# Optimization experiments

Measured on AMD Instinct MI355X. Metric: run time of the kernel, lower is better.

## Reference

```python
import jax, jax.numpy as jnp
import numpy as np

N = 50000
E = 1600000
D = 128
NUM_CLASSES = 10
SLOPE = 0.01  # torch leaky_relu default


def leaky_relu(x):
    return jnp.where(x >= 0, x, SLOPE * x)


def gcn_conv(x, src, dst, norm_out, norm_in, W, b):
    # DGL GraphConv, norm='both': D_out^{-1/2} A^T D_in^{-1/2} applied as
    # scale-src -> scatter-sum to dst -> scale-dst, then linear + bias.
    h = x * norm_out[:, None]                        # [N, D]
    agg = jax.ops.segment_sum(h[src], dst, num_segments=N)  # [N, D]
    agg = agg * norm_in[:, None]
    return agg @ W + b


def setup_inputs() -> dict:
    key = jax.random.key(0)
    ks = jax.random.split(key, 12)
    def w(k, shape, fan_in):
        return jax.random.normal(k, shape, dtype=jnp.float32) / np.sqrt(fan_in)
    return {
        "x": jax.random.normal(ks[0], (N, D), dtype=jnp.float32),
        "src": jax.random.randint(ks[1], (E,), 0, N),
        "dst": jax.random.randint(ks[2], (E,), 0, N),
        "W1": w(ks[3], (D, D), D),
        "b1": jnp.zeros((D,), jnp.float32),
        "W2": w(ks[4], (D, D), D),
        "b2": jnp.zeros((D,), jnp.float32),
        "agg_w": w(ks[5], (D, 1), D),
        "agg_b": jnp.zeros((1,), jnp.float32),
        "d1_w": w(ks[6], (N, 100), N),
        "d1_b": jnp.zeros((100,), jnp.float32),
        "d2_w": w(ks[7], (100, 20), 100),
        "d2_b": jnp.zeros((20,), jnp.float32),
        "d3_w": w(ks[8], (20, NUM_CLASSES), 20),
        "d3_b": jnp.zeros((NUM_CLASSES,), jnp.float32),
    }


def reference(x, src, dst, W1, b1, W2, b2, agg_w, agg_b,
              d1_w, d1_b, d2_w, d2_b, d3_w, d3_b):
    ones = jnp.ones((E,), jnp.float32)
    out_deg = jax.ops.segment_sum(ones, src, num_segments=N)
    in_deg = jax.ops.segment_sum(ones, dst, num_segments=N)
    # DGL clamps degrees to min 1 (allow_zero_in_degree path)
    norm_out = jnp.power(jnp.clip(out_deg, 1.0), -0.5)
    norm_in = jnp.power(jnp.clip(in_deg, 1.0), -0.5)

    h = gcn_conv(x, src, dst, norm_out, norm_in, W1, b1)
    h = leaky_relu(h)
    h = gcn_conv(h, src, dst, norm_out, norm_in, W2, b2)
    h = h @ agg_w + agg_b            # [N, 1]
    # dropout omitted (eval mode / identity)
    h = h.reshape(-1, N)             # [1, N]
    h = h @ d1_w + d1_b              # [1, 100]
    h = leaky_relu(h @ d2_w + d2_b)  # [1, 20]
    h = h @ d3_w + d3_b              # [1, num_classes]
    return h.reshape(1, -1)
```

## Files before the change

### kernel.cpp

```cpp
#include <hip/hip_runtime.h>
#include <hip/hip_bf16.h>

#define SLOPE 0.01f
#define D 128
#define CAP 64
#define NB 256
#define NPMAX 1024
#define ZB 512
#define ZIT 10

__device__ __forceinline__ float us2f(unsigned int u) {
    union { unsigned int i; float f; } c; c.i = u << 16; return c.f;
}
__device__ __forceinline__ unsigned int f2us(float f) {
    union { float f; unsigned int i; } c; c.f = f;
    return (c.i + 0x7fffu + ((c.i >> 16) & 1u)) >> 16;
}

__global__ void __launch_bounds__(256) k_hist782(const int* __restrict__ dst,
                                                 unsigned int* __restrict__ histg,
                                                 unsigned int* __restrict__ odeg,
                                                 int E, int NP, int N) {
    __shared__ int lb[NPMAX];
    int b = blockIdx.x;
    for (int i = b * 256 + threadIdx.x; i < N; i += NB * 256) odeg[i] = 0u;
    for (int i = threadIdx.x; i < NP; i += 256) lb[i] = 0;
    __syncthreads();
    int ch = (E + NB - 1) / NB;
    int e0 = b * ch, e1 = min(E, e0 + ch);
    for (int e = e0 + threadIdx.x; e < e1; e += 256) atomicAdd(&lb[dst[e] >> 6], 1);
    __syncthreads();
    unsigned int* row = histg + (size_t)b * NP;
    for (int i = threadIdx.x; i < NP; i += 256) row[i] = (unsigned int)lb[i];
}

__global__ void __launch_bounds__(NB) k_scanA(const unsigned int* __restrict__ histg,
                                              unsigned int* __restrict__ boffT,
                                              unsigned int* __restrict__ tot, int NP) {
    __shared__ int wsum[NB / 64];
    int p = blockIdx.x, tid = threadIdx.x, lane = tid & 63, w = tid >> 6;
    int val = (int)histg[(size_t)tid * NP + p];
    int sc = val;
    for (int off = 1; off < 64; off <<= 1) { int t = __shfl_up(sc, off, 64); if (lane >= off) sc += t; }
    if (lane == 63) wsum[w] = sc;
    __syncthreads();
    if (w == 0 && lane < NB / 64) {
        int v4 = wsum[lane];
        for (int off = 1; off < NB / 64; off <<= 1) { int t = __shfl_up(v4, off, 64); if (lane >= off) v4 += t; }
        wsum[lane] = v4;
    }
    __syncthreads();
    int excl = ((w == 0) ? 0 : wsum[w - 1]) + sc - val;
    boffT[(size_t)p * NB + tid] = (unsigned int)excl;
    if (tid == NB - 1) tot[p] = (unsigned int)(excl + val);
}

__global__ void __launch_bounds__(1024) k_misc(const unsigned int* __restrict__ tot,
                                               int* __restrict__ pbase, int NP,
                                               const float* __restrict__ W2, const float* __restrict__ b2,
                                               const float* __restrict__ agg_w, const float* __restrict__ agg_b,
                                               float* __restrict__ v, float* __restrict__ c) {
    __shared__ int wsum[16];
    __shared__ float aw[D];
    __shared__ float red[D];
    int tid = threadIdx.x;
    if (blockIdx.x == 0) {
        int lane = tid & 63, w = tid >> 6;
        int val = (tid < NP) ? (int)tot[tid] : 0;
        int sc = val;
        for (int off = 1; off < 64; off <<= 1) { int t = __shfl_up(sc, off, 64); if (lane >= off) sc += t; }
        if (lane == 63) wsum[w] = sc;
        __syncthreads();
        if (w == 0 && lane < 16) {
            int v16 = wsum[lane];
            for (int off = 1; off < 16; off <<= 1) { int t = __shfl_up(v16, off, 64); if (lane >= off) v16 += t; }
            wsum[lane] = v16;
        }
        __syncthreads();
        int excl = ((w == 0) ? 0 : wsum[w - 1]) + sc - val;
        if (tid <= NP) pbase[tid] = excl;
    } else {
        if (tid >= 128) return;
        aw[tid] = agg_w[tid];
        __syncthreads();
        float acc = 0.f;
        for (int j = 0; j < D; j++) acc += W2[tid * D + j] * aw[j];
        v[tid] = acc;
        red[tid] = b2[tid] * aw[tid];
        __syncthreads();
        for (int off = 64; off > 0; off >>= 1) {
            if (tid < off) red[tid] += red[tid + off];
            __syncthreads();
        }
        if (tid == 0) c[0] = red[0] + agg_b[0];
    }
}

__global__ void __launch_bounds__(256) k_psort(const int* __restrict__ src, const int* __restrict__ dst,
                                               const int* __restrict__ pbase,
                                               const unsigned int* __restrict__ boffT,
                                               unsigned int* __restrict__ parted,
                                               unsigned int* __restrict__ odeg, int E, int NP) {
    __shared__ unsigned int lbase[NPMAX];
    __shared__ int lcur[NPMAX];
    int b = blockIdx.x;
    for (int i = threadIdx.x; i < NP; i += 256) {
        lbase[i] = (unsigned int)pbase[i] + boffT[(size_t)i * NB + b];
        lcur[i] = 0;
    }
    __syncthreads();
    int ch = (E + NB - 1) / NB;
    int e0 = b * ch, e1 = min(E, e0 + ch);
    for (int e = e0 + threadIdx.x; e < e1; e += 256) {
        int d = dst[e], s = src[e];
        atomicAdd(&odeg[s], 1u);
        int p = d >> 6;
        int pos = atomicAdd(&lcur[p], 1);
        parted[lbase[p] + pos] = (unsigned int)s | ((unsigned int)(d & 63) << 16);
    }
}

__global__ void __launch_bounds__(256) k_bfill(
    const int* __restrict__ poff, const unsigned int* __restrict__ parted,
    unsigned short* __restrict__ bucket, int* __restrict__ cnt_in,
    float* __restrict__ norm_in, int N) {
    __shared__ int lcnt[64];
    __shared__ unsigned short blds[64 * CAP];
    int p = blockIdx.x, tid = threadIdx.x;
    if (tid < 64) lcnt[tid] = 0;
    __syncthreads();
    int e0 = poff[p], e1 = poff[p + 1];
    for (int i = e0 + tid; i < e1; i += 256) {
        unsigned int rec = parted[i];
        int dl = rec >> 16;
        int pos = atomicAdd(&lcnt[dl], 1);
        if (pos < CAP) blds[dl * CAP + pos] = (unsigned short)(rec & 0xffffu);
    }
    __syncthreads();
    int nmax = min(64, N - (p << 6));
    unsigned int* bg = (unsigned int*)(bucket + ((long)p << 6) * CAP);
    const unsigned int* bl = (const unsigned int*)blds;
    for (int i = tid; i < nmax * (CAP / 2); i += 256) bg[i] = bl[i];
    if (tid < nmax) {
        cnt_in[(p << 6) + tid] = lcnt[tid];
        norm_in[(p << 6) + tid] = rsqrtf(fmaxf((float)lcnt[tid], 1.0f));
    }
}

__global__ void k_prep(const float2* __restrict__ x2, const unsigned int* __restrict__ odeg,
                       unsigned int* __restrict__ xb, int total ) {
    int g = blockIdx.x * blockDim.x + threadIdx.x;
    if (g >= total) return;
    float no = rsqrtf(fmaxf((float)odeg[g >> 6], 1.0f));
    float2 p = x2[g];
    xb[g] = f2us(p.x * no) | (f2us(p.y * no) << 16);
}

__global__ void __launch_bounds__(256) k_gather1(
    const int* __restrict__ cnt_in, const unsigned short* __restrict__ bucket,
    const unsigned int* __restrict__ xb, unsigned int* __restrict__ agg, int N) {
    int b = blockIdx.x;
    int xcd = b & 7;
    int pass = xcd >> 1;
    int idx = ((b >> 3) << 1) + (xcd & 1);
    int tid = threadIdx.x;
    int node = idx * 4 + (tid >> 6);
    if (node >= N) return;
    int lane = tid & 63;
    int slot = lane >> 4;
    int fu = lane & 15;
    int deg = min(__builtin_nontemporal_load(cnt_in + node), CAP);
    int myedge = 0;
    if (lane < deg) myedge = (int)__builtin_nontemporal_load(bucket + (long)node * CAP + lane);
    const unsigned int* xq = xb + (size_t)(pass << 4) + fu;
    float ax = 0.f, ay = 0.f;
    {
        unsigned int pv[8];
#pragma unroll
        for (int i = 0; i < 8; i++) {
            int s = __shfl(myedge, i * 4 + slot, 64);
            pv[i] = xq[(size_t)s << 6];
        }
#pragma unroll
        for (int i = 0; i < 8; i++) {
            bool ok = (i * 4 + slot) < deg;
            ax += ok ? us2f(pv[i] & 0xffffu) : 0.f;
            ay += ok ? us2f(pv[i] >> 16) : 0.f;
        }
    }
    if (deg > 32) {
        unsigned int pv[8];
#pragma unroll
        for (int i = 0; i < 8; i++) {
            int s = __shfl(myedge, 32 + i * 4 + slot, 64);
            pv[i] = xq[(size_t)s << 6];
        }
#pragma unroll
        for (int i = 0; i < 8; i++) {
            bool ok = (32 + i * 4 + slot) < deg;
            ax += ok ? us2f(pv[i] & 0xffffu) : 0.f;
            ay += ok ? us2f(pv[i] >> 16) : 0.f;
        }
    }
    ax += __shfl_xor(ax, 16, 64); ay += __shfl_xor(ay, 16, 64);
    ax += __shfl_xor(ax, 32, 64); ay += __shfl_xor(ay, 32, 64);
    if (slot == 0)
        __builtin_nontemporal_store(f2us(ax) | (f2us(ay) << 16),
                                    agg + (long)node * 64 + (pass << 4) + fu);
}

__global__ void __launch_bounds__(256) k_lin1q(
    const unsigned int* __restrict__ agg, const float* __restrict__ W1,
    const float* __restrict__ b1, const float* __restrict__ v,
    const unsigned int* __restrict__ odeg, const float* __restrict__ norm_in,
    float* __restrict__ q, int N) {
    __shared__ __align__(16) unsigned int at[64 * 64];
    int tid = threadIdx.x;
    int cg = tid & 31;
    int rg = tid >> 5;
    int r0 = blockIdx.x * 64;

    {
        const uint4* ag4 = (const uint4*)agg;
        uint4* at4 = (uint4*)at;
        uint4 z4; z4.x = z4.y = z4.z = z4.w = 0u;
#pragma unroll
        for (int it = 0; it < 4; it++) {
            int idx = tid + it * 256;
            int r = idx >> 4;
            at4[idx] = (r0 + r < N) ? ag4[(long)(r0 + r) * 16 + (idx & 15)] : z4;
        }
    }
    __syncthreads();

    float4 acc[8];
#pragma unroll
    for (int i = 0; i < 8; i++) acc[i].x = acc[i].y = acc[i].z = acc[i].w = 0.f;

    const float4* W4 = (const float4*)W1;
    const uint4* a4 = ((const uint4*)at) + rg * 8 * 16;
    for (int kq = 0; kq < 16; kq++) {
        float4 w0 = W4[(kq * 8 + 0) * 32 + cg];
        float4 w1 = W4[(kq * 8 + 1) * 32 + cg];
        float4 w2 = W4[(kq * 8 + 2) * 32 + cg];
        float4 w3 = W4[(kq * 8 + 3) * 32 + cg];
        float4 w4 = W4[(kq * 8 + 4) * 32 + cg];
        float4 w5 = W4[(kq * 8 + 5) * 32 + cg];
        float4 w6 = W4[(kq * 8 + 6) * 32 + cg];
        float4 w7 = W4[(kq * 8 + 7) * 32 + cg];
#pragma unroll
        for (int i = 0; i < 8; i++) {
            uint4 a = a4[i * 16 + kq];
            float f0 = us2f(a.x & 0xffffu), f1 = us2f(a.x >> 16);
            float f2 = us2f(a.y & 0xffffu), f3 = us2f(a.y >> 16);
            float f4 = us2f(a.z & 0xffffu), f5 = us2f(a.z >> 16);
            float f6 = us2f(a.w & 0xffffu), f7 = us2f(a.w >> 16);
            acc[i].x += f0*w0.x + f1*w1.x + f2*w2.x + f3*w3.x + f4*w4.x + f5*w5.x + f6*w6.x + f7*w7.x;
            acc[i].y += f0*w0.y + f1*w1.y + f2*w2.y + f3*w3.y + f4*w4.y + f5*w5.y + f6*w6.y + f7*w7.y;
            acc[i].z += f0*w0.z + f1*w1.z + f2*w2.z + f3*w3.z + f4*w4.z + f5*w5.z + f6*w6.z + f7*w7.z;
            acc[i].w += f0*w0.w + f1*w1.w + f2*w2.w + f3*w3.w + f4*w4.w + f5*w5.w + f6*w6.w + f7*w7.w;
        }
    }

    float4 bv = ((const float4*)b1)[cg];
    float4 vv = ((const float4*)v)[cg];
#pragma unroll
    for (int i = 0; i < 8; i++) {
        int row = r0 + rg * 8 + i;
        bool valid = row < N;
        float ni = valid ? norm_in[row] : 0.f;
        float hx = ni * acc[i].x + bv.x; hx = hx >= 0.f ? hx : SLOPE * hx;
        float hy = ni * acc[i].y + bv.y; hy = hy >= 0.f ? hy : SLOPE * hy;
        float hz = ni * acc[i].z + bv.z; hz = hz >= 0.f ? hz : SLOPE * hz;
        float hw = ni * acc[i].w + bv.w; hw = hw >= 0.f ? hw : SLOPE * hw;
        float p = hx * vv.x + hy * vv.y + hz * vv.z + hw * vv.w;
        p += __shfl_down(p, 16, 32);
        p += __shfl_down(p, 8, 32);
        p += __shfl_down(p, 4, 32);
        p += __shfl_down(p, 2, 32);
        p += __shfl_down(p, 1, 32);
        if ((tid & 31) == 0 && valid)
            q[row] = rsqrtf(fmaxf((float)odeg[row], 1.0f)) * p;
    }
}

__global__ void __launch_bounds__(256) k_gather2(
    const int* __restrict__ cnt_in, const unsigned short* __restrict__ bucket,
    const float* __restrict__ q, const float* __restrict__ norm_in,
    const float* __restrict__ c, float* __restrict__ s, int N) {
    int tid = threadIdx.x;
    int node = blockIdx.x * 8 + (tid >> 5);
    int lane = tid & 31;
    if (node >= N) return;
    int deg = min(cnt_in[node], CAP);
    float t = 0.f;
    for (int j = lane; j < deg; j += 32) t += q[(int)bucket[(long)node * CAP + j]];
    t += __shfl_down(t, 16, 32);
    t += __shfl_down(t, 8, 32);
    t += __shfl_down(t, 4, 32);
    t += __shfl_down(t, 2, 32);
    t += __shfl_down(t, 1, 32);
    if (lane == 0) s[node] = norm_in[node] * t + c[0];
}

__global__ void __launch_bounds__(256) k_z1(const float* __restrict__ s,
                                            const float* __restrict__ d1w,
                                            float* __restrict__ zpart, int N) {
    __shared__ float ls[ZIT * 10];
    __shared__ float4 part[256];
    int tid = threadIdx.x;
    int qd = tid % 25;
    int rl = tid / 25;
    int rows_per = (N + gridDim.x - 1) / gridDim.x;
    int r0 = blockIdx.x * rows_per;
    int r1 = min(N, r0 + rows_per);
    if (tid < ZIT * 10) ls[tid] = (r0 + tid < r1) ? s[r0 + tid] : 0.f;
    __syncthreads();
    const float4* w4 = (const float4*)d1w;
    float4 acc; acc.x = acc.y = acc.z = acc.w = 0.f;
    if (tid < 250) {
#pragma unroll
        for (int it = 0; it < ZIT; it++) {
            int ro = rl + it * 10;
            float sv = ls[ro];
            int rr = min(r0 + ro, N - 1);
            float4 w = w4[(long)rr * 25 + qd];
            acc.x += sv * w.x; acc.y += sv * w.y; acc.z += sv * w.z; acc.w += sv * w.w;
        }
    }
    part[tid] = acc;
    __syncthreads();
    if (tid < 25) {
        float4 t = part[tid];
#pragma unroll
        for (int g = 1; g < 10; g++) {
            float4 p = part[tid + 25 * g];
            t.x += p.x; t.y += p.y; t.z += p.z; t.w += p.w;
        }
        ((float4*)zpart)[blockIdx.x * 25 + tid] = t;
    }
}

__global__ void __launch_bounds__(256) k_zred(const float* __restrict__ zpart,
                                              float* __restrict__ z1) {
    int gid = blockIdx.x * 256 + threadIdx.x;
    int col = gid >> 6;
    int lane = gid & 63;
    if (col >= 100) return;
    float sum = 0.f;
#pragma unroll
    for (int i = 0; i < ZB / 64; i++) {
        int b = lane * (ZB / 64) + i;
        sum += zpart[(size_t)b * 100 + col];
    }
    for (int off = 32; off > 0; off >>= 1) sum += __shfl_down(sum, off, 64);
    if (lane == 0) z1[col] = sum;
}

__global__ void k_head(const float* __restrict__ z1, const float* __restrict__ d1b,
                       const float* __restrict__ d2w, const float* __restrict__ d2b,
                       const float* __restrict__ d3w, const float* __restrict__ d3b,
                       float* __restrict__ out) {
    __shared__ float z1c[100];
    __shared__ float z2c[20];
    int tid = threadIdx.x;
    for (int i = tid; i < 100; i += 64) z1c[i] = z1[i] + d1b[i];
    __syncthreads();
    if (tid < 20) {
        float acc = d2b[tid];
        for (int k = 0; k < 100; k++) acc += z1c[k] * d2w[k * 20 + tid];
        z2c[tid] = acc >= 0.f ? acc : SLOPE * acc;
    }
    __syncthreads();
    if (tid < 10) {
        float acc = d3b[tid];
        for (int j = 0; j < 20; j++) acc += z2c[j] * d3w[j * 10 + tid];
        out[tid] = acc;
    }
}

extern "C" void kernel_launch(void* const* d_in, const int* in_sizes, int n_in,
                              void* d_out, int out_size, void* d_ws, size_t ws_size,
                              hipStream_t stream) {
    const int N = in_sizes[0] / D;
    const int E = in_sizes[1];
    const int NP = (N + 63) >> 6;

    const float* x     = (const float*)d_in[0];
    const int* src     = (const int*)d_in[1];
    const int* dst     = (const int*)d_in[2];
    const float* W1    = (const float*)d_in[3];
    const float* b1    = (const float*)d_in[4];
    const float* W2    = (const float*)d_in[5];
    const float* b2    = (const float*)d_in[6];
    const float* agg_w = (const float*)d_in[7];
    const float* agg_b = (const float*)d_in[8];
    const float* d1w   = (const float*)d_in[9];
    const float* d1b   = (const float*)d_in[10];
    const float* d2w   = (const float*)d_in[11];
    const float* d2b   = (const float*)d_in[12];
    const float* d3w   = (const float*)d_in[13];
    const float* d3b   = (const float*)d_in[14];
    float* out = (float*)d_out;

    unsigned int* xb  = (unsigned int*)d_ws;
    unsigned int* agg = xb + (size_t)N * 64;
    unsigned int* parted = agg;
    unsigned int* histg  = agg + E;
    unsigned int* boffT  = histg + (size_t)NB * NP;
    unsigned int* tot    = boffT + (size_t)NP * NB;
    unsigned int* odeg   = agg + (size_t)N * 64;
    float* norm_in    = (float*)(odeg + N);
    float* q          = norm_in + N;
    float* s          = q + N;
    float* v          = s + N;
    float* c          = v + 128;
    float* z1         = c + 4;
    int* pbase        = (int*)(z1 + 128);
    int* cnt_in       = pbase + NP + 16;
    unsigned short* bucket = (unsigned short*)(cnt_in + N);
    float* zpart      = (float*)(bucket + (size_t)N * CAP);


    k_hist782<<<NB, 256, 0, stream>>>(dst, histg, odeg, E, NP, N);
    k_scanA<<<NP, NB, 0, stream>>>(histg, boffT, tot, NP);
    k_misc<<<2, 1024, 0, stream>>>(tot, pbase, NP, W2, b2, agg_w, agg_b, v, c);
    k_psort<<<NB, 256, 0, stream>>>(src, dst, pbase, boffT, parted, odeg, E, NP);
    k_bfill<<<NP, 256, 0, stream>>>(pbase, parted, bucket, cnt_in, norm_in, N);
    k_prep<<<(N * 64 + 255) / 256, 256, 0, stream>>>((const float2*)x, odeg, xb, N * 64);

    {
        const int G = (N + 3) / 4;
        const int G2 = (G + 1) / 2;
        k_gather1<<<8 * G2, 256, 0, stream>>>(cnt_in, bucket, xb, agg, N);
    }
    k_lin1q<<<(N + 63) / 64, 256, 0, stream>>>(agg, W1, b1, v, odeg, norm_in, q, N);
    k_gather2<<<(N + 7) / 8, 256, 0, stream>>>(cnt_in, bucket, q, norm_in, c, s, N);
    k_z1<<<ZB, 256, 0, stream>>>(s, d1w, zpart, N);
    k_zred<<<25, 256, 0, stream>>>(zpart, z1);
    k_head<<<1, 64, 0, stream>>>(z1, d1b, d2w, d2b, d3w, d3b, out);
}
```

Baseline: 363.0 us.

## Split xb into per-pass planes with zero sentinel row and fuse tail kernels

The bf16 feature buffer is rearranged so each of the four 16-word feature passes has its own contiguous plane of N+1 rows, and an extra all-zero sentinel row is added. Bucket slots are pre-filled with the sentinel index, so the gather can drop its per-edge validity masks and the conditional bucket load. Each pass in k_gather1 now reads from a smaller contiguous plane, which is meant to improve cache locality. The zpart reduction and the MLP head are merged into one 1024-thread kernel, removing a launch. The cost is extra sentinel initialisation in k_bfill and gathers that always read the sentinel row for padded slots.

```diff
diff --git a/kernel.cpp b/kernel.cpp
--- a/kernel.cpp
+++ b/kernel.cpp
@@ -128,6 +128,8 @@
     __shared__ unsigned short blds[64 * CAP];
     int p = blockIdx.x, tid = threadIdx.x;
     if (tid < 64) lcnt[tid] = 0;
+    unsigned int sent2 = (unsigned int)N | ((unsigned int)N << 16);
+    for (int i = tid; i < 64 * CAP / 2; i += 256) ((unsigned int*)blds)[i] = sent2;
     __syncthreads();
     int e0 = poff[p], e1 = poff[p + 1];
     for (int i = e0 + tid; i < e1; i += 256) {
@@ -148,12 +150,19 @@
 }
 
 __global__ void k_prep(const float2* __restrict__ x2, const unsigned int* __restrict__ odeg,
-                       unsigned int* __restrict__ xb, int total ) {
+                       unsigned int* __restrict__ xb, int N) {
     int g = blockIdx.x * blockDim.x + threadIdx.x;
-    if (g >= total) return;
-    float no = rsqrtf(fmaxf((float)odeg[g >> 6], 1.0f));
-    float2 p = x2[g];
-    xb[g] = f2us(p.x * no) | (f2us(p.y * no) << 16);
+    int node = g >> 6;
+    if (node > N) return;
+    int u = g & 63;
+    int pass = u >> 4, fu = u & 15;
+    unsigned int outv = 0u;
+    if (node < N) {
+        float no = rsqrtf(fmaxf((float)odeg[node], 1.0f));
+        float2 p = x2[g];
+        outv = f2us(p.x * no) | (f2us(p.y * no) << 16);
+    }
+    xb[((size_t)pass * (N + 1) + node) * 16 + fu] = outv;
 }
 
 __global__ void __launch_bounds__(256) k_gather1(
@@ -170,22 +179,20 @@
     int slot = lane >> 4;
     int fu = lane & 15;
     int deg = min(__builtin_nontemporal_load(cnt_in + node), CAP);
-    int myedge = 0;
-    if (lane < deg) myedge = (int)__builtin_nontemporal_load(bucket + (long)node * CAP + lane);
-    const unsigned int* xq = xb + (size_t)(pass << 4) + fu;
+    int myedge = (int)__builtin_nontemporal_load(bucket + (long)node * CAP + lane);
+    const unsigned int* xq = xb + (size_t)pass * (N + 1) * 16 + fu;
     float ax = 0.f, ay = 0.f;
     {
         unsigned int pv[8];
 #pragma unroll
         for (int i = 0; i < 8; i++) {
             int s = __shfl(myedge, i * 4 + slot, 64);
-            pv[i] = xq[(size_t)s << 6];
+            pv[i] = xq[(size_t)s << 4];
         }
 #pragma unroll
         for (int i = 0; i < 8; i++) {
-            bool ok = (i * 4 + slot) < deg;
-            ax += ok ? us2f(pv[i] & 0xffffu) : 0.f;
-            ay += ok ? us2f(pv[i] >> 16) : 0.f;
+            ax += us2f(pv[i] & 0xffffu);
+            ay += us2f(pv[i] >> 16);
         }
     }
     if (deg > 32) {
@@ -193,13 +200,12 @@
 #pragma unroll
         for (int i = 0; i < 8; i++) {
             int s = __shfl(myedge, 32 + i * 4 + slot, 64);
-            pv[i] = xq[(size_t)s << 6];
+            pv[i] = xq[(size_t)s << 4];
         }
 #pragma unroll
         for (int i = 0; i < 8; i++) {
-            bool ok = (32 + i * 4 + slot) < deg;
-            ax += ok ? us2f(pv[i] & 0xffffu) : 0.f;
-            ay += ok ? us2f(pv[i] >> 16) : 0.f;
+            ax += us2f(pv[i] & 0xffffu);
+            ay += us2f(pv[i] >> 16);
         }
     }
     ax += __shfl_xor(ax, 16, 64); ay += __shfl_xor(ay, 16, 64);
@@ -341,30 +347,25 @@
     }
 }
 
-__global__ void __launch_bounds__(256) k_zred(const float* __restrict__ zpart,
-                                              float* __restrict__ z1) {
-    int gid = blockIdx.x * 256 + threadIdx.x;
-    int col = gid >> 6;
-    int lane = gid & 63;
-    if (col >= 100) return;
-    float sum = 0.f;
-#pragma unroll
-    for (int i = 0; i < ZB / 64; i++) {
-        int b = lane * (ZB / 64) + i;
-        sum += zpart[(size_t)b * 100 + col];
-    }
-    for (int off = 32; off > 0; off >>= 1) sum += __shfl_down(sum, off, 64);
-    if (lane == 0) z1[col] = sum;
-}
-
-__global__ void k_head(const float* __restrict__ z1, const float* __restrict__ d1b,
-                       const float* __restrict__ d2w, const float* __restrict__ d2b,
-                       const float* __restrict__ d3w, const float* __restrict__ d3b,
-                       float* __restrict__ out) {
+__global__ void __launch_bounds__(1024) k_tail(const float* __restrict__ zpart,
+                                               const float* __restrict__ d1b,
+                                               const float* __restrict__ d2w, const float* __restrict__ d2b,
+                                               const float* __restrict__ d3w, const float* __restrict__ d3b,
+                                               float* __restrict__ out) {
     __shared__ float z1c[100];
     __shared__ float z2c[20];
     int tid = threadIdx.x;
-    for (int i = tid; i < 100; i += 64) z1c[i] = z1[i] + d1b[i];
+    if (tid < 100) z1c[tid] = 0.f;
+    __syncthreads();
+    if (tid < 1000) {
+        int col = tid % 100;
+        int bg = tid / 100;
+        float acc = 0.f;
+        for (int b = bg; b < ZB; b += 10) acc += zpart[(size_t)b * 100 + col];
+        atomicAdd(&z1c[col], acc);
+    }
+    __syncthreads();
+    if (tid < 100) z1c[tid] += d1b[tid];
     __syncthreads();
     if (tid < 20) {
         float acc = d2b[tid];
@@ -404,7 +405,7 @@
     float* out = (float*)d_out;
 
     unsigned int* xb  = (unsigned int*)d_ws;
-    unsigned int* agg = xb + (size_t)N * 64;
+    unsigned int* agg = xb + (size_t)(N + 1) * 64;
     unsigned int* parted = agg;
     unsigned int* histg  = agg + E;
     unsigned int* boffT  = histg + (size_t)NB * NP;
@@ -415,8 +416,7 @@
     float* s          = q + N;
     float* v          = s + N;
     float* c          = v + 128;
-    float* z1         = c + 4;
-    int* pbase        = (int*)(z1 + 128);
+    int* pbase        = (int*)(c + 4);
     int* cnt_in       = pbase + NP + 16;
     unsigned short* bucket = (unsigned short*)(cnt_in + N);
     float* zpart      = (float*)(bucket + (size_t)N * CAP);
@@ -427,7 +427,7 @@
     k_misc<<<2, 1024, 0, stream>>>(tot, pbase, NP, W2, b2, agg_w, agg_b, v, c);
     k_psort<<<NB, 256, 0, stream>>>(src, dst, pbase, boffT, parted, odeg, E, NP);
     k_bfill<<<NP, 256, 0, stream>>>(pbase, parted, bucket, cnt_in, norm_in, N);
-    k_prep<<<(N * 64 + 255) / 256, 256, 0, stream>>>((const float2*)x, odeg, xb, N * 64);
+    k_prep<<<((N + 1) * 64 + 255) / 256, 256, 0, stream>>>((const float2*)x, odeg, xb, N);
 
     {
         const int G = (N + 3) / 4;
@@ -437,6 +437,5 @@
     k_lin1q<<<(N + 63) / 64, 256, 0, stream>>>(agg, W1, b1, v, odeg, norm_in, q, N);
     k_gather2<<<(N + 7) / 8, 256, 0, stream>>>(cnt_in, bucket, q, norm_in, c, s, N);
     k_z1<<<ZB, 256, 0, stream>>>(s, d1w, zpart, N);
-    k_zred<<<25, 256, 0, stream>>>(zpart, z1);
-    k_head<<<1, 64, 0, stream>>>(z1, d1b, d2w, d2b, d3w, d3b, out);
-}
+    k_tail<<<1, 1024, 0, stream>>>(zpart, d1b, d2w, d2b, d3w, d3b, out);
+}
```

After: 353.5 us. 1.03x faster.
